# Kernel tuning notes

Measured on AMD Instinct MI355X. Metric: run time of the kernel, lower is better.

## Reference

```python
import jax, jax.numpy as jnp
import numpy as np

D_MODEL = 1024
D_STATE = 16
D_CONV = 4
EXPAND = 2
D_INNER = EXPAND * D_MODEL          # 2048
DT_RANK = (D_MODEL + 15) // 16      # 64 (mamba 'auto')
B, L = 2, 1024


def _mamba_params(key, scale=0.02):
    ks = jax.random.split(key, 6)
    return dict(
        inW=jax.random.normal(ks[0], (2 * D_INNER, D_MODEL), jnp.float32) * scale,
        convW=jax.random.normal(ks[1], (D_INNER, 1, D_CONV), jnp.float32) * scale,
        convb=jnp.zeros((D_INNER,), jnp.float32),
        xprojW=jax.random.normal(ks[2], (DT_RANK + 2 * D_STATE, D_INNER), jnp.float32) * scale,
        dtW=jax.random.normal(ks[3], (D_INNER, DT_RANK), jnp.float32) * scale,
        dtb=jax.random.normal(ks[4], (D_INNER,), jnp.float32) * scale,
        A_log=jnp.log(jnp.tile(jnp.arange(1, D_STATE + 1, dtype=jnp.float32), (D_INNER, 1))),
        Dskip=jnp.ones((D_INNER,), jnp.float32),
        outW=jax.random.normal(ks[5], (D_MODEL, D_INNER), jnp.float32) * scale,
    )


def setup_inputs() -> dict:
    key = jax.random.key(0)
    kx, kf, kb, kp = jax.random.split(key, 4)
    inp = {"x": jax.random.normal(kx, (B, L, D_MODEL), jnp.float32)}
    inp["ln_w"] = jnp.ones((D_MODEL,), jnp.float32)
    inp["ln_b"] = jnp.zeros((D_MODEL,), jnp.float32)
    for pref, k in (("f_", kf), ("b_", kb)):
        for name, v in _mamba_params(k).items():
            inp[pref + name] = v
    inp["proj_W"] = jax.random.normal(kp, (D_MODEL, 2 * D_MODEL), jnp.float32) * 0.02
    inp["proj_b"] = jnp.zeros((D_MODEL,), jnp.float32)
    return inp


def _layernorm(x, w, b, eps=1e-5):
    mu = jnp.mean(x, axis=-1, keepdims=True)
    var = jnp.var(x, axis=-1, keepdims=True)
    return (x - mu) * jax.lax.rsqrt(var + eps) * w + b


def _mamba(x, inW, convW, convb, xprojW, dtW, dtb, A_log, Dskip, outW):
    # x: [B, L, d_model]
    xz = jnp.einsum('bld,ed->ble', x, inW)           # [B,L,2*d_inner]
    xs, z = jnp.split(xz, 2, axis=-1)                # each [B,L,d_inner]
    # depthwise causal conv over L
    xc = jnp.transpose(xs, (0, 2, 1))                # [B,d_inner,L]
    xc = jax.lax.conv_general_dilated(
        xc, convW, window_strides=(1,), padding=[(D_CONV - 1, 0)],
        feature_group_count=D_INNER)
    xs = jax.nn.silu(jnp.transpose(xc + convb[None, :, None], (0, 2, 1)))
    # input-dependent dt, B, C
    xdb = jnp.einsum('bld,ed->ble', xs, xprojW)      # [B,L,dt_rank+2*d_state]
    dt, Bm, Cm = jnp.split(xdb, [DT_RANK, DT_RANK + D_STATE], axis=-1)
    dt = jax.nn.softplus(jnp.einsum('blr,dr->bld', dt, dtW) + dtb)  # [B,L,d_inner]
    A = -jnp.exp(A_log)                              # [d_inner,d_state], negative
    dA = jnp.exp(dt[..., None] * A)                  # [B,L,d_inner,d_state]
    dBx = dt[..., None] * Bm[:, :, None, :] * xs[..., None]

    def step(h, inputs):
        dA_t, dBx_t, C_t = inputs                    # [B,d,s],[B,d,s],[B,s]
        h = h * dA_t + dBx_t
        y = jnp.einsum('bds,bs->bd', h, C_t)
        return h, y

    h0 = jnp.zeros((x.shape[0], D_INNER, D_STATE), x.dtype)
    _, ys = jax.lax.scan(step, h0, (jnp.moveaxis(dA, 1, 0),
                                    jnp.moveaxis(dBx, 1, 0),
                                    jnp.moveaxis(Cm, 1, 0)))
    y = jnp.moveaxis(ys, 0, 1)                       # [B,L,d_inner]
    y = (y + xs * Dskip) * jax.nn.silu(z)
    return jnp.einsum('bld,ed->ble', y, outW)        # [B,L,d_model]


def reference(x, ln_w, ln_b,
              f_inW, f_convW, f_convb, f_xprojW, f_dtW, f_dtb, f_A_log, f_Dskip, f_outW,
              b_inW, b_convW, b_convb, b_xprojW, b_dtW, b_dtb, b_A_log, b_Dskip, b_outW,
              proj_W, proj_b):
    normed = _layernorm(x, ln_w, ln_b)
    fwd_out = _mamba(normed, f_inW, f_convW, f_convb, f_xprojW, f_dtW, f_dtb,
                     f_A_log, f_Dskip, f_outW)
    bwd_out = _mamba(normed[:, ::-1, :], b_inW, b_convW, b_convb, b_xprojW, b_dtW,
                     b_dtb, b_A_log, b_Dskip, b_outW)[:, ::-1, :]
    combined = jnp.concatenate([fwd_out, bwd_out], axis=-1)
    return x + jnp.einsum('blc,ec->ble', combined, proj_W) + proj_b
```

## Files before the change

### kernel.cpp

```cpp
#include <hip/hip_runtime.h>
#include <hip/hip_bf16.h>
#include <math.h>

#define DM   1024
#define DI   2048
#define DTR  64
#define DST  16
#define NB   2
#define LL   1024
#define MR   (NB*LL)
#define XLD  128
#define KS   8

typedef __bf16 bf16x8 __attribute__((ext_vector_type(8)));
typedef float  f32x4  __attribute__((ext_vector_type(4)));

__device__ __forceinline__ float siluf(float x) { return x / (1.f + __expf(-x)); }
__device__ __forceinline__ float softplusf(float x) {
    return fmaxf(x, 0.f) + log1pf(__expf(-fabsf(x)));
}
__device__ __forceinline__ unsigned short f2bf(float f) {
    __hip_bfloat16 h = __float2bfloat16(f);
    return *reinterpret_cast<unsigned short*>(&h);
}
__device__ __forceinline__ float bf2f(__hip_bfloat16 h) { return __bfloat162float(h); }

__device__ __forceinline__ void gl2lds16(const __hip_bfloat16* g, __hip_bfloat16* l)
{
    __builtin_amdgcn_global_load_lds(
        (const __attribute__((address_space(1))) unsigned int*)g,
        (__attribute__((address_space(3))) unsigned int*)l, 16, 0, 0);
}

__global__ __launch_bounds__(256) void prep_k(
    const float* __restrict__ s0, const float* __restrict__ s1,
    const float* __restrict__ s2, const float* __restrict__ s3,
    const float* __restrict__ s4, __hip_bfloat16* __restrict__ warena,
    const float* __restrict__ fx, const float* __restrict__ bx,
    __hip_bfloat16* __restrict__ wpb2,
    const float* __restrict__ fo, const float* __restrict__ bo,
    __hip_bfloat16* __restrict__ wot,
    const float* __restrict__ x, const float* __restrict__ lnw,
    const float* __restrict__ lnb, __hip_bfloat16* __restrict__ nb)
{
    __shared__ float pshm[64 * 65];
    const int b = blockIdx.x;
    const int tid = threadIdx.x;

    if (b < 10496) {
        long idx = (long)b * 1024 + tid * 4;
        const float* src; long off;
        if      (idx <  4194304L) { src = s0; off = idx; }
        else if (idx <  8388608L) { src = s1; off = idx -  4194304L; }
        else if (idx < 10485760L) { src = s2; off = idx -  8388608L; }
        else if (idx < 10616832L) { src = s3; off = idx - 10485760L; }
        else                      { src = s4; off = idx - 10616832L; }
        float4 v = *(const float4*)(src + off);
        ushort4 o;
        o.x = f2bf(v.x); o.y = f2bf(v.y); o.z = f2bf(v.z); o.w = f2bf(v.w);
        *(ushort4*)((unsigned short*)warena + idx) = o;
    } else if (b < 10624) {
        int t = b - 10496;
        int z = t >> 6;
        const float* in = z ? bx : fx;
        int idx = ((t & 63) * 256 + tid) * 4;
        int row = idx >> 11;
        ushort4 o = make_ushort4(0, 0, 0, 0);
        if (row < 96) {
            float4 v = *(const float4*)(in + idx);
            o.x = f2bf(v.x); o.y = f2bf(v.y); o.z = f2bf(v.z); o.w = f2bf(v.w);
        }
        *(ushort4*)((unsigned short*)wpb2 + (size_t)z * 128 * DI + idx) = o;
    } else if (b < 11648) {
        int t = b - 10624;
        int z = t >> 9; t &= 511;
        const float* src = z ? bo : fo;
        int c0 = (t & 31) * 64;
        int r0 = (t >> 5) * 64;
        int tc = tid & 63;
        int tr = tid >> 6;
        #pragma unroll
        for (int ii = 0; ii < 16; ++ii) {
            int rl = tr + ii * 4;
            pshm[tc * 65 + rl] = src[(size_t)(r0 + rl) * DI + c0 + tc];
        }
        __syncthreads();
        __hip_bfloat16* dst = wot + (size_t)z * DI * DM;
        #pragma unroll
        for (int ii = 0; ii < 16; ++ii) {
            int cl = tr + ii * 4;
            dst[(size_t)(c0 + cl) * DM + r0 + tc] = __float2bfloat16(pshm[cl * 65 + tc]);
        }
    } else {
        int row = b - 11648;
        const float* xr = x + (size_t)row * DM;
        float4 v = *(const float4*)(xr + tid * 4);
        float s = v.x + v.y + v.z + v.w;
        float q = v.x*v.x + v.y*v.y + v.z*v.z + v.w*v.w;
        #pragma unroll
        for (int off = 32; off > 0; off >>= 1) {
            s += __shfl_xor(s, off, 64);
            q += __shfl_xor(q, off, 64);
        }
        int wv = tid >> 6;
        if ((tid & 63) == 0) { pshm[wv] = s; pshm[8 + wv] = q; }
        __syncthreads();
        s = pshm[0] + pshm[1] + pshm[2] + pshm[3];
        q = pshm[8] + pshm[9] + pshm[10] + pshm[11];
        float mu  = s * (1.f / DM);
        float var = q * (1.f / DM) - mu * mu;
        float rstd = rsqrtf(var + 1e-5f);
        float4 wv4 = *(const float4*)(lnw + tid * 4);
        float4 bv4 = *(const float4*)(lnb + tid * 4);
        ushort4 o;
        o.x = f2bf((v.x - mu) * rstd * wv4.x + bv4.x);
        o.y = f2bf((v.y - mu) * rstd * wv4.y + bv4.y);
        o.z = f2bf((v.z - mu) * rstd * wv4.z + bv4.z);
        o.w = f2bf((v.w - mu) * rstd * wv4.w + bv4.w);
        *(ushort4*)((unsigned short*)nb + (size_t)row * DM + tid * 4) = o;
    }
}

template<int EPI>
__global__ __launch_bounds__(256) void gemm_gl(
    const __hip_bfloat16* __restrict__ A, int lda, size_t aofs,
    const __hip_bfloat16* __restrict__ B, int ldb, size_t bofs,
    void* __restrict__ Cp, int ldc, size_t cofs, int K,
    const float* __restrict__ bias0, const float* __restrict__ bias1)
{
    __shared__ __hip_bfloat16 smem[2 * 128 * 64];
    __hip_bfloat16* As = smem;
    __hip_bfloat16* Bs = smem + 128 * 64;
    const int tid  = threadIdx.x;
    const int z    = blockIdx.z;
    const int bm   = blockIdx.y * 128;
    const int bn   = blockIdx.x * 128;
    const __hip_bfloat16* Az = A + (size_t)z * aofs;
    const __hip_bfloat16* Bz = B + (size_t)z * bofs;
    const int wv   = tid >> 6;
    const int lane = tid & 63;
    const int wr   = (wv >> 1) * 64;
    const int wc   = (wv & 1) * 64;
    const int srow = wv * 32 + (lane >> 3);
    const int cg   = ((lane & 7) ^ (lane >> 3)) * 8;
    const int fr   = lane & 15;
    const int quad = lane >> 4;
    const int pc0  = (quad ^ (fr & 7)) * 8;
    const int pc1  = ((4 + quad) ^ (fr & 7)) * 8;

    f32x4 acc[4][4] = {};

    for (int k0 = 0; k0 < K; k0 += 64) {
        __syncthreads();
        #pragma unroll
        for (int i = 0; i < 4; ++i) {
            int r = srow + i * 8;
            gl2lds16(Az + (size_t)(bm + r) * lda + k0 + cg, As + wv * 2048 + i * 512);
            gl2lds16(Bz + (size_t)(bn + r) * ldb + k0 + cg, Bs + wv * 2048 + i * 512);
        }
        __syncthreads();
        #pragma unroll
        for (int kk = 0; kk < 2; ++kk) {
            const int pc = kk ? pc1 : pc0;
            bf16x8 af[4], bf_[4];
            #pragma unroll
            for (int i = 0; i < 4; ++i) {
                af[i]  = *(const bf16x8*)(As + (wr + i * 16 + fr) * 64 + pc);
                bf_[i] = *(const bf16x8*)(Bs + (wc + i * 16 + fr) * 64 + pc);
            }
            #pragma unroll
            for (int i = 0; i < 4; ++i)
                #pragma unroll
                for (int j = 0; j < 4; ++j)
                    acc[i][j] = __builtin_amdgcn_mfma_f32_16x16x32_bf16(
                        af[i], bf_[j], acc[i][j], 0, 0, 0);
        }
    }

    const float* bias = (EPI == 3) ? (z ? bias1 : bias0) : nullptr;
    float* eps = (float*)smem;
    const int half = wv >> 1;
    const int lrow = tid >> 3;
    const int cseg = (tid & 7) * 16;
    const int gr_  = bm + (lrow >> 4) * 64 + (lrow & 15);
    #pragma unroll
    for (int i = 0; i < 4; ++i) {
        __syncthreads();
        #pragma unroll
        for (int j = 0; j < 4; ++j)
            #pragma unroll
            for (int r = 0; r < 4; ++r)
                eps[(half * 16 + quad * 4 + r) * 132 + wc + j * 16 + fr] = acc[i][j][r];
        __syncthreads();
        float vals[16];
        *(float4*)(vals +  0) = *(const float4*)(eps + lrow * 132 + cseg +  0);
        *(float4*)(vals +  4) = *(const float4*)(eps + lrow * 132 + cseg +  4);
        *(float4*)(vals +  8) = *(const float4*)(eps + lrow * 132 + cseg +  8);
        *(float4*)(vals + 12) = *(const float4*)(eps + lrow * 132 + cseg + 12);
        int gr = gr_ + i * 16;
        int gc = bn + cseg;
        if (EPI == 0) {
            float* dst = (float*)Cp + (size_t)z * cofs + (size_t)gr * ldc + gc;
            *(float4*)(dst +  0) = *(const float4*)(vals +  0);
            *(float4*)(dst +  4) = *(const float4*)(vals +  4);
            *(float4*)(dst +  8) = *(const float4*)(vals +  8);
            *(float4*)(dst + 12) = *(const float4*)(vals + 12);
        } else {
            unsigned short os[16];
            #pragma unroll
            for (int c = 0; c < 16; ++c) {
                float t = vals[c];
                if (EPI == 3) t = softplusf(t + bias[gc + c]);
                os[c] = f2bf(t);
            }
            unsigned short* dst = (unsigned short*)Cp + (size_t)z * cofs +
                                  (size_t)gr * ldc + gc;
            *(ushort4*)(dst +  0) = *(ushort4*)(os +  0);
            *(ushort4*)(dst +  4) = *(ushort4*)(os +  4);
            *(ushort4*)(dst +  8) = *(ushort4*)(os +  8);
            *(ushort4*)(dst + 12) = *(ushort4*)(os + 12);
        }
    }
}

__global__ __launch_bounds__(256) void xproj_part_k(
    const __hip_bfloat16* __restrict__ A,
    const __hip_bfloat16* __restrict__ B,
    float* __restrict__ part)
{
    __shared__ __hip_bfloat16 smem[2 * 128 * 64];
    __hip_bfloat16* As = smem;
    __hip_bfloat16* Bs = smem + 128 * 64;
    const int tid  = threadIdx.x;
    const int ks   = blockIdx.x;
    const int bm   = blockIdx.y * 128;
    const int z    = blockIdx.z;
    const __hip_bfloat16* Az = A + (size_t)z * MR * DI;
    const __hip_bfloat16* Bz = B + (size_t)z * 128 * DI;
    const int kb   = ks * (DI / KS);
    const int wv   = tid >> 6;
    const int lane = tid & 63;
    const int wr   = (wv >> 1) * 64;
    const int wc   = (wv & 1) * 64;
    const int srow = wv * 32 + (lane >> 3);
    const int cg   = ((lane & 7) ^ (lane >> 3)) * 8;
    const int fr   = lane & 15;
    const int quad = lane >> 4;
    const int pc0  = (quad ^ (fr & 7)) * 8;
    const int pc1  = ((4 + quad) ^ (fr & 7)) * 8;

    f32x4 acc[4][4] = {};

    #pragma unroll
    for (int k0 = 0; k0 < DI / KS; k0 += 64) {
        __syncthreads();
        #pragma unroll
        for (int i = 0; i < 4; ++i) {
            int r = srow + i * 8;
            gl2lds16(Az + (size_t)(bm + r) * DI + kb + k0 + cg, As + wv * 2048 + i * 512);
            gl2lds16(Bz + (size_t)r * DI + kb + k0 + cg,        Bs + wv * 2048 + i * 512);
        }
        __syncthreads();
        #pragma unroll
        for (int kk = 0; kk < 2; ++kk) {
            const int pc = kk ? pc1 : pc0;
            bf16x8 af[4], bf_[4];
            #pragma unroll
            for (int i = 0; i < 4; ++i) {
                af[i]  = *(const bf16x8*)(As + (wr + i * 16 + fr) * 64 + pc);
                bf_[i] = *(const bf16x8*)(Bs + (wc + i * 16 + fr) * 64 + pc);
            }
            #pragma unroll
            for (int i = 0; i < 4; ++i)
                #pragma unroll
                for (int j = 0; j < 4; ++j)
                    acc[i][j] = __builtin_amdgcn_mfma_f32_16x16x32_bf16(
                        af[i], bf_[j], acc[i][j], 0, 0, 0);
        }
    }

    float* dst = part + ((size_t)z * KS + ks) * MR * XLD;
    const int er = quad * 4;
    #pragma unroll
    for (int i = 0; i < 4; ++i)
        #pragma unroll
        for (int j = 0; j < 4; ++j) {
            int row = bm + wr + i * 16 + er;
            int col = wc + j * 16 + fr;
            #pragma unroll
            for (int r = 0; r < 4; ++r)
                dst[(size_t)(row + r) * XLD + col] = acc[i][j][r];
        }
}

__global__ __launch_bounds__(256) void xproj_reduce_k(
    const float* __restrict__ part, float* __restrict__ xdb,
    __hip_bfloat16* __restrict__ xdbt)
{
    int z = blockIdx.y;
    size_t idx = ((size_t)blockIdx.x * 256 + threadIdx.x) * 4;
    const float* p = part + (size_t)z * KS * MR * XLD;
    float4 s = make_float4(0.f, 0.f, 0.f, 0.f);
    #pragma unroll
    for (int ks = 0; ks < KS; ++ks) {
        float4 v = *(const float4*)(p + (size_t)ks * MR * XLD + idx);
        s.x += v.x; s.y += v.y; s.z += v.z; s.w += v.w;
    }
    *(float4*)(xdb + (size_t)z * MR * XLD + idx) = s;
    int c = (int)(idx & (XLD - 1));
    if (c < 64) {
        size_t m = idx >> 7;
        ushort4 o;
        o.x = f2bf(s.x); o.y = f2bf(s.y); o.z = f2bf(s.z); o.w = f2bf(s.w);
        *(ushort4*)((unsigned short*)xdbt + (size_t)z * MR * 64 + m * 64 + c) = o;
    }
}

__global__ __launch_bounds__(256) void conv_silu_k(
    const __hip_bfloat16* __restrict__ xz2,
    const float* __restrict__ fW, const float* __restrict__ fb,
    const float* __restrict__ bW, const float* __restrict__ bb_,
    __hip_bfloat16* __restrict__ xsb2)
{
    int dirv = blockIdx.y;
    int idx = blockIdx.x * 256 + threadIdx.x;
    int d = idx & (DI - 1);
    int m = idx >> 11;
    int t = m & (LL - 1);
    int bb = m >> 10;
    const float* w  = (dirv ? bW : fW) + d * 4;
    const __hip_bfloat16* xz = xz2 + (size_t)dirv * MR * 2 * DI;
    float acc = (dirv ? bb_ : fb)[d];
    if (dirv == 0) {
        #pragma unroll
        for (int k = 0; k < 4; ++k) {
            int tt = t - 3 + k;
            if (tt >= 0)
                acc = fmaf(w[k], bf2f(xz[(size_t)(bb * LL + tt) * (2 * DI) + d]), acc);
        }
    } else {
        #pragma unroll
        for (int k = 0; k < 4; ++k) {
            int tt = t + 3 - k;
            if (tt < LL)
                acc = fmaf(w[k], bf2f(xz[(size_t)(bb * LL + tt) * (2 * DI) + d]), acc);
        }
    }
    xsb2[(size_t)dirv * MR * DI + (size_t)m * DI + d] = __float2bfloat16(siluf(acc));
}

__global__ __launch_bounds__(256) void scan1_k(
    const __hip_bfloat16* __restrict__ dtf2, const __hip_bfloat16* __restrict__ xsb2,
    const float* __restrict__ xdb2,
    const float* __restrict__ fA, const float* __restrict__ bA,
    float* __restrict__ hend, float* __restrict__ aprod, int G, int Cn)
{
    int d  = blockIdx.x * 256 + threadIdx.x;
    int bb = blockIdx.y;
    int zz = blockIdx.z;
    int dirv = (zz >= G) ? 1 : 0;
    int g = zz - (dirv ? G : 0);
    const float* A_log = dirv ? bA : fA;
    const __hip_bfloat16* dtf = dtf2 + (size_t)dirv * MR * DI;
    const __hip_bfloat16* xs = xsb2 + (size_t)dirv * MR * DI;
    const float* xdb = xdb2 + (size_t)dirv * MR * XLD;
    size_t hoff = (size_t)dirv * G * (NB * DI * DST);

    float Ad[DST], h[DST], ap[DST];
    bool pw = true;
    #pragma unroll
    for (int s = 0; s < DST; ++s) {
        Ad[s] = -__expf(A_log[d * DST + s]);
        pw = pw && (fabsf(Ad[s] + (float)(s + 1)) < 1e-3f * (s + 1));
        h[s] = 0.f; ap[s] = 1.f;
    }
    int i0 = g * Cn;
    for (int i = 0; i < Cn; ++i) {
        int ii = i0 + i;
        int t = dirv ? (LL - 1 - ii) : ii;
        size_t m = (size_t)bb * LL + t;
        float dtv = bf2f(dtf[m * DI + d]);
        float xv  = bf2f(xs[m * DI + d]);
        const float* bc = xdb + m * XLD;
        float dtx = dtv * xv;
        float dAv[DST];
        if (pw) {
            float r = __expf(-dtv);
            float a = r;
            #pragma unroll
            for (int s = 0; s < DST; ++s) { dAv[s] = a; a *= r; }
        } else {
            #pragma unroll
            for (int s = 0; s < DST; ++s) dAv[s] = __expf(dtv * Ad[s]);
        }
        #pragma unroll
        for (int s = 0; s < DST; ++s) {
            h[s] = fmaf(h[s], dAv[s], dtx * bc[64 + s]);
            ap[s] *= dAv[s];
        }
    }
    size_t base = hoff + ((size_t)(g * NB + bb) * DI + d) * DST;
    #pragma unroll
    for (int s = 0; s < DST; s += 4) {
        *(float4*)(hend  + base + s) = make_float4(h[s], h[s+1], h[s+2], h[s+3]);
        *(float4*)(aprod + base + s) = make_float4(ap[s], ap[s+1], ap[s+2], ap[s+3]);
    }
}

__global__ __launch_bounds__(256) void scan2_k(
    float* __restrict__ hend, const float* __restrict__ aprod, int G)
{
    int dirv = blockIdx.y;
    int idx = blockIdx.x * 256 + threadIdx.x;
    const int slab = NB * DI * DST;
    size_t hoff = (size_t)dirv * G * slab;
    float carry = 0.f;
    for (int g = 0; g < G; ++g) {
        size_t off = hoff + (size_t)g * slab + idx;
        float a = aprod[off];
        float e = hend[off];
        hend[off] = carry;
        carry = fmaf(a, carry, e);
    }
}

__global__ __launch_bounds__(256) void scan3_k(
    const __hip_bfloat16* __restrict__ dtf2, const __hip_bfloat16* __restrict__ xsb2,
    const float* __restrict__ xdb2, const __hip_bfloat16* __restrict__ xz2,
    const float* __restrict__ fA, const float* __restrict__ bA,
    const float* __restrict__ fD, const float* __restrict__ bD,
    const float* __restrict__ hin, __hip_bfloat16* __restrict__ ycat, int G, int Cn)
{
    int d  = blockIdx.x * 256 + threadIdx.x;
    int bb = blockIdx.y;
    int zz = blockIdx.z;
    int dirv = (zz >= G) ? 1 : 0;
    int g = zz - (dirv ? G : 0);
    const float* A_log = dirv ? bA : fA;
    const float* Dskip = dirv ? bD : fD;
    const __hip_bfloat16* dtf = dtf2 + (size_t)dirv * MR * DI;
    const __hip_bfloat16* xs = xsb2 + (size_t)dirv * MR * DI;
    const float* xdb = xdb2 + (size_t)dirv * MR * XLD;
    const __hip_bfloat16* xz = xz2 + (size_t)dirv * MR * 2 * DI;
    size_t hoff = (size_t)dirv * G * (NB * DI * DST);

    float Ad[DST], h[DST];
    bool pw = true;
    size_t base = hoff + ((size_t)(g * NB + bb) * DI + d) * DST;
    #pragma unroll
    for (int s = 0; s < DST; ++s) {
        Ad[s] = -__expf(A_log[d * DST + s]);
        pw = pw && (fabsf(Ad[s] + (float)(s + 1)) < 1e-3f * (s + 1));
        h[s] = hin[base + s];
    }
    float Dsk = Dskip[d];
    int i0 = g * Cn;
    for (int i = 0; i < Cn; ++i) {
        int ii = i0 + i;
        int t = dirv ? (LL - 1 - ii) : ii;
        size_t m = (size_t)bb * LL + t;
        float dtv = bf2f(dtf[m * DI + d]);
        float xv  = bf2f(xs[m * DI + d]);
        const float* bc = xdb + m * XLD;
        float dtx = dtv * xv;
        float dAv[DST];
        if (pw) {
            float r = __expf(-dtv);
            float a = r;
            #pragma unroll
            for (int s = 0; s < DST; ++s) { dAv[s] = a; a *= r; }
        } else {
            #pragma unroll
            for (int s = 0; s < DST; ++s) dAv[s] = __expf(dtv * Ad[s]);
        }
        float yv = 0.f;
        #pragma unroll
        for (int s = 0; s < DST; ++s) {
            h[s] = fmaf(h[s], dAv[s], dtx * bc[64 + s]);
            yv = fmaf(h[s], bc[80 + s], yv);
        }
        float zv = bf2f(xz[m * (2 * DI) + DI + d]);
        ycat[m * (2 * DI) + (size_t)dirv * DI + d] =
            __float2bfloat16((yv + xv * Dsk) * siluf(zv));
    }
}

__global__ __launch_bounds__(256) void scan_mono_k(
    const __hip_bfloat16* __restrict__ dtf2, const __hip_bfloat16* __restrict__ xsb2,
    const float* __restrict__ xdb2, const __hip_bfloat16* __restrict__ xz2,
    const float* __restrict__ fA, const float* __restrict__ bA,
    const float* __restrict__ fD, const float* __restrict__ bD,
    __hip_bfloat16* __restrict__ ycat)
{
    int d  = blockIdx.x * 256 + threadIdx.x;
    int bb = blockIdx.y;
    int dirv = blockIdx.z;
    const float* A_log = dirv ? bA : fA;
    const float* Dskip = dirv ? bD : fD;
    const __hip_bfloat16* dtf = dtf2 + (size_t)dirv * MR * DI;
    const __hip_bfloat16* xs = xsb2 + (size_t)dirv * MR * DI;
    const float* xdb = xdb2 + (size_t)dirv * MR * XLD;
    const __hip_bfloat16* xz = xz2 + (size_t)dirv * MR * 2 * DI;
    float Ad[DST], h[DST];
    #pragma unroll
    for (int s = 0; s < DST; ++s) { Ad[s] = -__expf(A_log[d * DST + s]); h[s] = 0.f; }
    float Dsk = Dskip[d];
    for (int i = 0; i < LL; ++i) {
        int t = dirv ? (LL - 1 - i) : i;
        size_t m = (size_t)bb * LL + t;
        float dtv = bf2f(dtf[m * DI + d]);
        float xv  = bf2f(xs[m * DI + d]);
        const float* bc = xdb + m * XLD;
        float dtx = dtv * xv;
        float yv = 0.f;
        #pragma unroll
        for (int s = 0; s < DST; ++s) {
            float dA = __expf(dtv * Ad[s]);
            h[s] = fmaf(h[s], dA, dtx * bc[64 + s]);
            yv = fmaf(h[s], bc[80 + s], yv);
        }
        float zv = bf2f(xz[m * (2 * DI) + DI + d]);
        ycat[m * (2 * DI) + (size_t)dirv * DI + d] =
            __float2bfloat16((yv + xv * Dsk) * siluf(zv));
    }
}

__global__ __launch_bounds__(256) void final_reduce_k(
    const float* __restrict__ part, const float* __restrict__ x,
    const float* __restrict__ proj_b, float* __restrict__ out)
{
    size_t idx = ((size_t)blockIdx.x * 256 + threadIdx.x) * 4;
    float4 s = make_float4(0.f, 0.f, 0.f, 0.f);
    #pragma unroll
    for (int z = 0; z < 4; ++z) {
        float4 v = *(const float4*)(part + (size_t)z * MR * DM + idx);
        s.x += v.x; s.y += v.y; s.z += v.z; s.w += v.w;
    }
    float4 xv = *(const float4*)(x + idx);
    float4 pb = *(const float4*)(proj_b + (idx & (DM - 1)));
    float4 o;
    o.x = xv.x + pb.x + s.x;
    o.y = xv.y + pb.y + s.y;
    o.z = xv.z + pb.z + s.z;
    o.w = xv.w + pb.w + s.w;
    *(float4*)(out + idx) = o;
}

extern "C" void kernel_launch(void* const* d_in, const int* in_sizes, int n_in,
                              void* d_out, int out_size, void* d_ws, size_t ws_size,
                              hipStream_t stream)
{
    const float* x      = (const float*)d_in[0];
    const float* ln_w   = (const float*)d_in[1];
    const float* ln_b   = (const float*)d_in[2];
    const float* f_inW    = (const float*)d_in[3];
    const float* f_convW  = (const float*)d_in[4];
    const float* f_convb  = (const float*)d_in[5];
    const float* f_xprojW = (const float*)d_in[6];
    const float* f_dtW    = (const float*)d_in[7];
    const float* f_dtb    = (const float*)d_in[8];
    const float* f_A_log  = (const float*)d_in[9];
    const float* f_Dskip  = (const float*)d_in[10];
    const float* f_outW   = (const float*)d_in[11];
    const float* b_inW    = (const float*)d_in[12];
    const float* b_convW  = (const float*)d_in[13];
    const float* b_convb  = (const float*)d_in[14];
    const float* b_xprojW = (const float*)d_in[15];
    const float* b_dtW    = (const float*)d_in[16];
    const float* b_dtb    = (const float*)d_in[17];
    const float* b_A_log  = (const float*)d_in[18];
    const float* b_Dskip  = (const float*)d_in[19];
    const float* b_outW   = (const float*)d_in[20];
    const float* proj_W = (const float*)d_in[21];
    const float* proj_b = (const float*)d_in[22];

    float* ws = (float*)d_ws;
    size_t o = 0;
    __hip_bfloat16* xz2  = (__hip_bfloat16*)(ws + o);
    __hip_bfloat16* wot  = xz2;
    float* fpart = ws + o;
    o += (size_t)2 * MR * 2 * DI / 2;
    __hip_bfloat16* xsb2 = (__hip_bfloat16*)(ws + o); o += (size_t)2 * MR * DI / 2;
    __hip_bfloat16* ycat = (__hip_bfloat16*)(ws + o);
    float* xpart = ws + o;
    o += (size_t)MR * 2 * DI / 2;
    float* xdb2 = ws + o; o += (size_t)2 * MR * XLD;
    __hip_bfloat16* xdbt = (__hip_bfloat16*)(ws + o); o += (size_t)2 * MR * 64 / 2;
    __hip_bfloat16* dtfb = (__hip_bfloat16*)(ws + o); o += (size_t)2 * MR * DI / 2;
    __hip_bfloat16* nb = (__hip_bfloat16*)(ws + o); o += (size_t)MR * DM / 2;
    __hip_bfloat16* warena = (__hip_bfloat16*)(ws + o); o += 15466496 / 2;
    float* hbuf = ws + o;
    size_t base_floats = o;

    __hip_bfloat16* wbi  = warena;
    __hip_bfloat16* pwb  = warena +  8388608;
    __hip_bfloat16* wdt  = warena + 10485760;
    __hip_bfloat16* wpb2 = warena + 10747904;
    __hip_bfloat16* wcat = warena + 11272192;

    const size_t slab = (size_t)NB * DI * DST;
    int G = 32;
    while (G > 4 && (base_floats + 4ull * G * slab) * 4 > ws_size) G >>= 1;
    int useChunks = ((base_floats + 4ull * G * slab) * 4 <= ws_size);
    float* hend  = hbuf;
    float* aprod = hbuf + 2ull * G * slab;
    int Cn = useChunks ? LL / G : LL;

    prep_k<<<13696, 256, 0, stream>>>(
        f_inW, b_inW, proj_W, f_dtW, b_dtW, warena,
        f_xprojW, b_xprojW, wpb2,
        f_outW, b_outW, wot,
        x, ln_w, ln_b, nb);

    gemm_gl<1><<<dim3(DI / 128, DM / 128, 2), 256, 0, stream>>>(
        pwb, 2 * DM, (size_t)DM, wot, DM, (size_t)DI * DM,
        wcat, 2 * DI, (size_t)DI, DM, nullptr, nullptr);

    gemm_gl<1><<<dim3((2 * DI) / 128, MR / 128, 2), 256, 0, stream>>>(
        nb, DM, 0, wbi, DM, (size_t)2 * DI * DM,
        xz2, 2 * DI, (size_t)MR * 2 * DI, DM, nullptr, nullptr);

    conv_silu_k<<<dim3((MR * DI) / 256, 2), 256, 0, stream>>>(
        xz2, f_convW, f_convb, b_convW, b_convb, xsb2);

    xproj_part_k<<<dim3(KS, MR / 128, 2), 256, 0, stream>>>(xsb2, wpb2, xpart);
    xproj_reduce_k<<<dim3((MR * XLD) / 1024, 2), 256, 0, stream>>>(xpart, xdb2, xdbt);

    gemm_gl<3><<<dim3(DI / 128, MR / 128, 2), 256, 0, stream>>>(
        xdbt, 64, (size_t)MR * 64, wdt, 64, (size_t)DI * 64,
        dtfb, DI, (size_t)MR * DI, 64, f_dtb, b_dtb);

    if (useChunks) {
        scan1_k<<<dim3(DI / 256, NB, 2 * G), 256, 0, stream>>>(
            dtfb, xsb2, xdb2, f_A_log, b_A_log, hend, aprod, G, Cn);
        scan2_k<<<dim3((NB * DI * DST) / 256, 2), 256, 0, stream>>>(hend, aprod, G);
        scan3_k<<<dim3(DI / 256, NB, 2 * G), 256, 0, stream>>>(
            dtfb, xsb2, xdb2, xz2, f_A_log, b_A_log, f_Dskip, b_Dskip,
            hend, ycat, G, Cn);
    } else {
        scan_mono_k<<<dim3(DI / 256, NB, 2), 256, 0, stream>>>(
            dtfb, xsb2, xdb2, xz2, f_A_log, b_A_log, f_Dskip, b_Dskip, ycat);
    }

    gemm_gl<0><<<dim3(DM / 128, MR / 128, 4), 256, 0, stream>>>(
        ycat, 2 * DI, 1024, wcat, 2 * DI, 1024,
        fpart, DM, (size_t)MR * DM, 1024, nullptr, nullptr);

    final_reduce_k<<<(MR * DM) / 1024, 256, 0, stream>>>(
        fpart, x, proj_b, (float*)d_out);
}
```

Before: 422.6 us.

## Fuse post-prep pipeline into one cooperative persistent kernel with grid syncs

Replaces the sequence of separate kernel launches (in-proj and weight-combine GEMMs, conv, x-proj split-K and reduce, dt GEMM, three scan phases, output GEMM and reduce) with a single cooperative persistent kernel that loops over virtual blocks and uses grid.sync between stages. The aim is to remove per-launch overhead and the idle gaps between dependent kernels. The in-proj GEMM and the weight-combine GEMM now run in the same stage, and the wot buffer is moved into hbuf so the two can run together. The cost is a grid capped at 512 blocks, so the scan phases and small stages may be underparallelised, plus the overhead of the grid barriers themselves. A fallback multi-kernel path that uses a fused inproj_wcat kernel is kept.

Result: slower. 900.3 us (+113.0%).

```diff
diff --git a/kernel.cpp b/kernel.cpp
--- a/kernel.cpp
+++ b/kernel.cpp
@@ -1,6 +1,9 @@
 #include <hip/hip_runtime.h>
 #include <hip/hip_bf16.h>
+#include <hip/hip_cooperative_groups.h>
 #include <math.h>
+
+namespace cg = cooperative_groups;
 
 #define DM   1024
 #define DI   2048
@@ -24,12 +27,321 @@
     return *reinterpret_cast<unsigned short*>(&h);
 }
 __device__ __forceinline__ float bf2f(__hip_bfloat16 h) { return __bfloat162float(h); }
+__device__ __forceinline__ float u2f(unsigned short u) {
+    return __uint_as_float(((unsigned int)u) << 16);
+}
 
 __device__ __forceinline__ void gl2lds16(const __hip_bfloat16* g, __hip_bfloat16* l)
 {
     __builtin_amdgcn_global_load_lds(
         (const __attribute__((address_space(1))) unsigned int*)g,
         (__attribute__((address_space(3))) unsigned int*)l, 16, 0, 0);
+}
+
+
+template<int EPI>
+__device__ __forceinline__ void gemm_tile(
+    __hip_bfloat16* smem, int tid,
+    const __hip_bfloat16* __restrict__ Az, int lda,
+    const __hip_bfloat16* __restrict__ Bz, int ldb,
+    void* __restrict__ Cz, int ldc, int K,
+    int bm, int bn, const float* __restrict__ bias)
+{
+    __hip_bfloat16* As = smem;
+    __hip_bfloat16* Bs = smem + 128 * 64;
+    const int wv   = tid >> 6;
+    const int lane = tid & 63;
+    const int wr   = (wv >> 1) * 64;
+    const int wc   = (wv & 1) * 64;
+    const int srow = wv * 32 + (lane >> 3);
+    const int cg_  = ((lane & 7) ^ (lane >> 3)) * 8;
+    const int fr   = lane & 15;
+    const int quad = lane >> 4;
+    const int pc0  = (quad ^ (fr & 7)) * 8;
+    const int pc1  = ((4 + quad) ^ (fr & 7)) * 8;
+
+    f32x4 acc[4][4] = {};
+
+    for (int k0 = 0; k0 < K; k0 += 64) {
+        __syncthreads();
+        #pragma unroll
+        for (int i = 0; i < 4; ++i) {
+            int r = srow + i * 8;
+            gl2lds16(Az + (size_t)(bm + r) * lda + k0 + cg_, As + wv * 2048 + i * 512);
+            gl2lds16(Bz + (size_t)(bn + r) * ldb + k0 + cg_, Bs + wv * 2048 + i * 512);
+        }
+        __syncthreads();
+        #pragma unroll
+        for (int kk = 0; kk < 2; ++kk) {
+            const int pc = kk ? pc1 : pc0;
+            bf16x8 af[4], bf_[4];
+            #pragma unroll
+            for (int i = 0; i < 4; ++i) {
+                af[i]  = *(const bf16x8*)(As + (wr + i * 16 + fr) * 64 + pc);
+                bf_[i] = *(const bf16x8*)(Bs + (wc + i * 16 + fr) * 64 + pc);
+            }
+            #pragma unroll
+            for (int i = 0; i < 4; ++i)
+                #pragma unroll
+                for (int j = 0; j < 4; ++j)
+                    acc[i][j] = __builtin_amdgcn_mfma_f32_16x16x32_bf16(
+                        af[i], bf_[j], acc[i][j], 0, 0, 0);
+        }
+    }
+
+    float* eps = (float*)smem;
+    const int half = wv >> 1;
+    const int lrow = tid >> 3;
+    const int cseg = (tid & 7) * 16;
+    const int gr_  = bm + (lrow >> 4) * 64 + (lrow & 15);
+    #pragma unroll
+    for (int i = 0; i < 4; ++i) {
+        __syncthreads();
+        #pragma unroll
+        for (int j = 0; j < 4; ++j)
+            #pragma unroll
+            for (int r = 0; r < 4; ++r)
+                eps[(half * 16 + quad * 4 + r) * 132 + wc + j * 16 + fr] = acc[i][j][r];
+        __syncthreads();
+        float vals[16];
+        *(float4*)(vals +  0) = *(const float4*)(eps + lrow * 132 + cseg +  0);
+        *(float4*)(vals +  4) = *(const float4*)(eps + lrow * 132 + cseg +  4);
+        *(float4*)(vals +  8) = *(const float4*)(eps + lrow * 132 + cseg +  8);
+        *(float4*)(vals + 12) = *(const float4*)(eps + lrow * 132 + cseg + 12);
+        int gr = gr_ + i * 16;
+        int gc = bn + cseg;
+        if (EPI == 0) {
+            float* dst = (float*)Cz + (size_t)gr * ldc + gc;
+            *(float4*)(dst +  0) = *(const float4*)(vals +  0);
+            *(float4*)(dst +  4) = *(const float4*)(vals +  4);
+            *(float4*)(dst +  8) = *(const float4*)(vals +  8);
+            *(float4*)(dst + 12) = *(const float4*)(vals + 12);
+        } else {
+            unsigned short os[16];
+            #pragma unroll
+            for (int c = 0; c < 16; ++c) {
+                float t = vals[c];
+                if (EPI == 3) t = softplusf(t + bias[gc + c]);
+                os[c] = f2bf(t);
+            }
+            unsigned short* dst = (unsigned short*)Cz + (size_t)gr * ldc + gc;
+            *(ushort4*)(dst +  0) = *(ushort4*)(os +  0);
+            *(ushort4*)(dst +  4) = *(ushort4*)(os +  4);
+            *(ushort4*)(dst +  8) = *(ushort4*)(os +  8);
+            *(ushort4*)(dst + 12) = *(ushort4*)(os + 12);
+        }
+    }
+}
+
+__device__ __forceinline__ void conv_body(
+    int q, const __hip_bfloat16* __restrict__ xz2,
+    const float* __restrict__ fW, const float* __restrict__ fb,
+    const float* __restrict__ bW, const float* __restrict__ bb_,
+    __hip_bfloat16* __restrict__ xsb2)
+{
+    const int TQH = MR * DI / 4;
+    int dirv = q >= TQH;
+    int mq = q - (dirv ? TQH : 0);
+    int m = mq >> 9;
+    int d = (mq & 511) << 2;
+    int t = m & (LL - 1);
+    int bb = m >> 10;
+    const float* W  = (dirv ? bW : fW) + d * 4;
+    const float* Bp = (dirv ? bb_ : fb) + d;
+    const __hip_bfloat16* xz = xz2 + (size_t)dirv * MR * 2 * DI;
+    float4 bi = *(const float4*)Bp;
+    float acc0 = bi.x, acc1 = bi.y, acc2 = bi.z, acc3 = bi.w;
+    float w_[16];
+    *(float4*)(w_ + 0)  = *(const float4*)(W + 0);
+    *(float4*)(w_ + 4)  = *(const float4*)(W + 4);
+    *(float4*)(w_ + 8)  = *(const float4*)(W + 8);
+    *(float4*)(w_ + 12) = *(const float4*)(W + 12);
+    #pragma unroll
+    for (int k = 0; k < 4; ++k) {
+        int tt = dirv ? (t + 3 - k) : (t - 3 + k);
+        bool ok = dirv ? (tt < LL) : (tt >= 0);
+        if (ok) {
+            ushort4 xv = *(const ushort4*)((const unsigned short*)xz +
+                         (size_t)(bb * LL + tt) * 2 * DI + d);
+            acc0 = fmaf(w_[0 + k],  u2f(xv.x), acc0);
+            acc1 = fmaf(w_[4 + k],  u2f(xv.y), acc1);
+            acc2 = fmaf(w_[8 + k],  u2f(xv.z), acc2);
+            acc3 = fmaf(w_[12 + k], u2f(xv.w), acc3);
+        }
+    }
+    ushort4 o;
+    o.x = f2bf(siluf(acc0)); o.y = f2bf(siluf(acc1));
+    o.z = f2bf(siluf(acc2)); o.w = f2bf(siluf(acc3));
+    *(ushort4*)((unsigned short*)xsb2 + (size_t)dirv * MR * DI +
+                (size_t)m * DI + d) = o;
+}
+
+__device__ __forceinline__ void xreduce_body(
+    size_t idx, int z, const float* __restrict__ part,
+    float* __restrict__ xdb, __hip_bfloat16* __restrict__ xdbt)
+{
+    const float* p = part + (size_t)z * KS * MR * XLD;
+    float4 s = make_float4(0.f, 0.f, 0.f, 0.f);
+    #pragma unroll
+    for (int ks = 0; ks < KS; ++ks) {
+        float4 v = *(const float4*)(p + (size_t)ks * MR * XLD + idx);
+        s.x += v.x; s.y += v.y; s.z += v.z; s.w += v.w;
+    }
+    *(float4*)(xdb + (size_t)z * MR * XLD + idx) = s;
+    int c = (int)(idx & (XLD - 1));
+    if (c < 64) {
+        size_t m = idx >> 7;
+        ushort4 o;
+        o.x = f2bf(s.x); o.y = f2bf(s.y); o.z = f2bf(s.z); o.w = f2bf(s.w);
+        *(ushort4*)((unsigned short*)xdbt + (size_t)z * MR * 64 + m * 64 + c) = o;
+    }
+}
+
+__device__ __forceinline__ void scan1_body(
+    int d, int bb, int dirv, int g, int G, int Cn,
+    const __hip_bfloat16* __restrict__ dtf2, const __hip_bfloat16* __restrict__ xsb2,
+    const float* __restrict__ xdb2,
+    const float* __restrict__ fA, const float* __restrict__ bA,
+    float* __restrict__ hend, float* __restrict__ aprod)
+{
+    const float* A_log = dirv ? bA : fA;
+    const __hip_bfloat16* dtf = dtf2 + (size_t)dirv * MR * DI;
+    const __hip_bfloat16* xs = xsb2 + (size_t)dirv * MR * DI;
+    const float* xdb = xdb2 + (size_t)dirv * MR * XLD;
+    size_t hoff = (size_t)dirv * G * (NB * DI * DST);
+
+    float Ad[DST], h[DST], ap[DST];
+    bool pw = true;
+    #pragma unroll
+    for (int s = 0; s < DST; ++s) {
+        Ad[s] = -__expf(A_log[d * DST + s]);
+        pw = pw && (fabsf(Ad[s] + (float)(s + 1)) < 1e-3f * (s + 1));
+        h[s] = 0.f; ap[s] = 1.f;
+    }
+    int i0 = g * Cn;
+    for (int i = 0; i < Cn; ++i) {
+        int ii = i0 + i;
+        int t = dirv ? (LL - 1 - ii) : ii;
+        size_t m = (size_t)bb * LL + t;
+        float dtv = bf2f(dtf[m * DI + d]);
+        float xv  = bf2f(xs[m * DI + d]);
+        const float* bc = xdb + m * XLD;
+        float dtx = dtv * xv;
+        float dAv[DST];
+        if (pw) {
+            float r = __expf(-dtv);
+            float a = r;
+            #pragma unroll
+            for (int s = 0; s < DST; ++s) { dAv[s] = a; a *= r; }
+        } else {
+            #pragma unroll
+            for (int s = 0; s < DST; ++s) dAv[s] = __expf(dtv * Ad[s]);
+        }
+        #pragma unroll
+        for (int s = 0; s < DST; ++s) {
+            h[s] = fmaf(h[s], dAv[s], dtx * bc[64 + s]);
+            ap[s] *= dAv[s];
+        }
+    }
+    size_t base = hoff + ((size_t)(g * NB + bb) * DI + d) * DST;
+    #pragma unroll
+    for (int s = 0; s < DST; s += 4) {
+        *(float4*)(hend  + base + s) = make_float4(h[s], h[s+1], h[s+2], h[s+3]);
+        *(float4*)(aprod + base + s) = make_float4(ap[s], ap[s+1], ap[s+2], ap[s+3]);
+    }
+}
+
+__device__ __forceinline__ void scan2_body(
+    int idx, int dirv, float* __restrict__ hend,
+    const float* __restrict__ aprod, int G)
+{
+    const int slab = NB * DI * DST;
+    size_t hoff = (size_t)dirv * G * slab;
+    float carry = 0.f;
+    for (int g = 0; g < G; ++g) {
+        size_t off = hoff + (size_t)g * slab + idx;
+        float a = aprod[off];
+        float e = hend[off];
+        hend[off] = carry;
+        carry = fmaf(a, carry, e);
+    }
+}
+
+__device__ __forceinline__ void scan3_body(
+    int d, int bb, int dirv, int g, int G, int Cn,
+    const __hip_bfloat16* __restrict__ dtf2, const __hip_bfloat16* __restrict__ xsb2,
+    const float* __restrict__ xdb2, const __hip_bfloat16* __restrict__ xz2,
+    const float* __restrict__ fA, const float* __restrict__ bA,
+    const float* __restrict__ fD, const float* __restrict__ bD,
+    const float* __restrict__ hin, __hip_bfloat16* __restrict__ ycat)
+{
+    const float* A_log = dirv ? bA : fA;
+    const float* Dskip = dirv ? bD : fD;
+    const __hip_bfloat16* dtf = dtf2 + (size_t)dirv * MR * DI;
+    const __hip_bfloat16* xs = xsb2 + (size_t)dirv * MR * DI;
+    const float* xdb = xdb2 + (size_t)dirv * MR * XLD;
+    const __hip_bfloat16* xz = xz2 + (size_t)dirv * MR * 2 * DI;
+    size_t hoff = (size_t)dirv * G * (NB * DI * DST);
+
+    float Ad[DST], h[DST];
+    bool pw = true;
+    size_t base = hoff + ((size_t)(g * NB + bb) * DI + d) * DST;
+    #pragma unroll
+    for (int s = 0; s < DST; ++s) {
+        Ad[s] = -__expf(A_log[d * DST + s]);
+        pw = pw && (fabsf(Ad[s] + (float)(s + 1)) < 1e-3f * (s + 1));
+        h[s] = hin[base + s];
+    }
+    float Dsk = Dskip[d];
+    int i0 = g * Cn;
+    for (int i = 0; i < Cn; ++i) {
+        int ii = i0 + i;
+        int t = dirv ? (LL - 1 - ii) : ii;
+        size_t m = (size_t)bb * LL + t;
+        float dtv = bf2f(dtf[m * DI + d]);
+        float xv  = bf2f(xs[m * DI + d]);
+        const float* bc = xdb + m * XLD;
+        float dtx = dtv * xv;
+        float dAv[DST];
+        if (pw) {
+            float r = __expf(-dtv);
+            float a = r;
+            #pragma unroll
+            for (int s = 0; s < DST; ++s) { dAv[s] = a; a *= r; }
+        } else {
+            #pragma unroll
+            for (int s = 0; s < DST; ++s) dAv[s] = __expf(dtv * Ad[s]);
+        }
+        float yv = 0.f;
+        #pragma unroll
+        for (int s = 0; s < DST; ++s) {
+            h[s] = fmaf(h[s], dAv[s], dtx * bc[64 + s]);
+            yv = fmaf(h[s], bc[80 + s], yv);
+        }
+        float zv = bf2f(xz[m * (2 * DI) + DI + d]);
+        ycat[m * (2 * DI) + (size_t)dirv * DI + d] =
+            __float2bfloat16((yv + xv * Dsk) * siluf(zv));
+    }
+}
+
+__device__ __forceinline__ void freduce_body(
+    size_t idx, const float* __restrict__ part, const float* __restrict__ x,
+    const float* __restrict__ proj_b, float* __restrict__ out)
+{
+    float4 s = make_float4(0.f, 0.f, 0.f, 0.f);
+    #pragma unroll
+    for (int z = 0; z < 4; ++z) {
+        float4 v = *(const float4*)(part + (size_t)z * MR * DM + idx);
+        s.x += v.x; s.y += v.y; s.z += v.z; s.w += v.w;
+    }
+    float4 xv = *(const float4*)(x + idx);
+    float4 pb = *(const float4*)(proj_b + (idx & (DM - 1)));
+    float4 o;
+    o.x = xv.x + pb.x + s.x;
+    o.y = xv.y + pb.y + s.y;
+    o.z = xv.z + pb.z + s.z;
+    o.w = xv.w + pb.w + s.w;
+    *(float4*)(out + idx) = o;
 }
 
 __global__ __launch_bounds__(256) void prep_k(
@@ -121,6 +433,114 @@
     }
 }
 
+struct MegaArgs {
+    const __hip_bfloat16 *nb, *wbi, *pwb, *wot, *wpb2, *wdt;
+    __hip_bfloat16 *xz2, *wcat, *xsb2, *xdbt, *dtfb, *ycat;
+    const float *fW, *fb, *bW, *bb_;
+    float *xpart, *xdb2;
+    const float *fdtb, *bdtb, *fA, *bA, *fD, *bD;
+    float *hend, *aprod;
+    const float *x, *proj_b;
+    float *fpart, *outp;
+    int G, Cn;
+};
+
+__global__ __launch_bounds__(256, 2) void mega_k(MegaArgs P)
+{
+    __shared__ __hip_bfloat16 smem[2 * 128 * 64];
+    cg::grid_group grid = cg::this_grid();
+    const int tid = threadIdx.x;
+    const int bid = blockIdx.x;
+    const int gsz = gridDim.x;
+
+    for (int vb = bid; vb < 1280; vb += gsz) {
+        const __hip_bfloat16 *Az, *Bz; __hip_bfloat16* Cz; int lda, bm, bn;
+        if (vb < 1024) {
+            int zz = vb >> 9, rem = vb & 511;
+            bm = (rem >> 5) * 128; bn = (rem & 31) * 128;
+            Az = P.nb; lda = DM;
+            Bz = P.wbi + (size_t)zz * 2 * DI * DM;
+            Cz = P.xz2 + (size_t)zz * MR * 2 * DI;
+        } else {
+            int w = vb - 1024; int zc = w >> 7, rem = w & 127;
+            bm = (rem >> 4) * 128; bn = (rem & 15) * 128;
+            Az = P.pwb + (size_t)zc * DM; lda = 2 * DM;
+            Bz = P.wot + (size_t)zc * DI * DM;
+            Cz = P.wcat + (size_t)zc * DI;
+        }
+        gemm_tile<1>(smem, tid, Az, lda, Bz, DM, Cz, 2 * DI, DM, bm, bn, nullptr);
+    }
+    grid.sync();
+
+    for (int vb = bid; vb < 8192; vb += gsz)
+        conv_body(vb * 256 + tid, P.xz2, P.fW, P.fb, P.bW, P.bb_, P.xsb2);
+    grid.sync();
+
+    for (int vb = bid; vb < 256; vb += gsz) {
+        int ks = vb & 7, byv = (vb >> 3) & 15, z = vb >> 7;
+        int kb = ks * (DI / KS);
+        gemm_tile<0>(smem, tid,
+            P.xsb2 + (size_t)z * MR * DI + kb, DI,
+            P.wpb2 + (size_t)z * 128 * DI + kb, DI,
+            P.xpart + ((size_t)z * KS + ks) * MR * XLD, XLD,
+            DI / KS, byv * 128, 0, nullptr);
+    }
+    grid.sync();
+
+    for (int vb = bid; vb < 512; vb += gsz)
+        xreduce_body(((size_t)(vb & 255) * 256 + tid) * 4, vb >> 8,
+                     P.xpart, P.xdb2, P.xdbt);
+    grid.sync();
+
+    for (int vb = bid; vb < 512; vb += gsz) {
+        int z = vb >> 8, rem = vb & 255;
+        int bm = (rem >> 4) * 128, bn = (rem & 15) * 128;
+        gemm_tile<3>(smem, tid,
+            P.xdbt + (size_t)z * MR * 64, 64,
+            P.wdt + (size_t)z * DI * 64, 64,
+            P.dtfb + (size_t)z * MR * DI, DI,
+            64, bm, bn, z ? P.bdtb : P.fdtb);
+    }
+    grid.sync();
+
+    for (int vb = bid; vb < 32 * P.G; vb += gsz) {
+        int zz = vb >> 4, bb = (vb >> 3) & 1, bx = vb & 7;
+        int dirv = (zz >= P.G) ? 1 : 0;
+        int g = zz - (dirv ? P.G : 0);
+        scan1_body(bx * 256 + tid, bb, dirv, g, P.G, P.Cn,
+                   P.dtfb, P.xsb2, P.xdb2, P.fA, P.bA, P.hend, P.aprod);
+    }
+    grid.sync();
+
+    for (int vb = bid; vb < 512; vb += gsz)
+        scan2_body((vb & 255) * 256 + tid, vb >> 8, P.hend, P.aprod, P.G);
+    grid.sync();
+
+    for (int vb = bid; vb < 32 * P.G; vb += gsz) {
+        int zz = vb >> 4, bb = (vb >> 3) & 1, bx = vb & 7;
+        int dirv = (zz >= P.G) ? 1 : 0;
+        int g = zz - (dirv ? P.G : 0);
+        scan3_body(bx * 256 + tid, bb, dirv, g, P.G, P.Cn,
+                   P.dtfb, P.xsb2, P.xdb2, P.xz2, P.fA, P.bA, P.fD, P.bD,
+                   P.hend, P.ycat);
+    }
+    grid.sync();
+
+    for (int vb = bid; vb < 512; vb += gsz) {
+        int z = vb >> 7, rem = vb & 127;
+        int bm = (rem >> 3) * 128, bn = (rem & 7) * 128;
+        gemm_tile<0>(smem, tid,
+            P.ycat + (size_t)z * 1024, 2 * DI,
+            P.wcat + (size_t)z * 1024, 2 * DI,
+            P.fpart + (size_t)z * MR * DM, DM,
+            1024, bm, bn, nullptr);
+    }
+    grid.sync();
+
+    for (int vb = bid; vb < 2048; vb += gsz)
+        freduce_body(((size_t)vb * 256 + tid) * 4, P.fpart, P.x, P.proj_b, P.outp);
+}
+
 template<int EPI>
 __global__ __launch_bounds__(256) void gemm_gl(
     const __hip_bfloat16* __restrict__ A, int lda, size_t aofs,
@@ -129,98 +549,38 @@
     const float* __restrict__ bias0, const float* __restrict__ bias1)
 {
     __shared__ __hip_bfloat16 smem[2 * 128 * 64];
-    __hip_bfloat16* As = smem;
-    __hip_bfloat16* Bs = smem + 128 * 64;
-    const int tid  = threadIdx.x;
-    const int z    = blockIdx.z;
-    const int bm   = blockIdx.y * 128;
-    const int bn   = blockIdx.x * 128;
-    const __hip_bfloat16* Az = A + (size_t)z * aofs;
-    const __hip_bfloat16* Bz = B + (size_t)z * bofs;
-    const int wv   = tid >> 6;
-    const int lane = tid & 63;
-    const int wr   = (wv >> 1) * 64;
-    const int wc   = (wv & 1) * 64;
-    const int srow = wv * 32 + (lane >> 3);
-    const int cg   = ((lane & 7) ^ (lane >> 3)) * 8;
-    const int fr   = lane & 15;
-    const int quad = lane >> 4;
-    const int pc0  = (quad ^ (fr & 7)) * 8;
-    const int pc1  = ((4 + quad) ^ (fr & 7)) * 8;
-
-    f32x4 acc[4][4] = {};
-
-    for (int k0 = 0; k0 < K; k0 += 64) {
-        __syncthreads();
-        #pragma unroll
-        for (int i = 0; i < 4; ++i) {
-            int r = srow + i * 8;
-            gl2lds16(Az + (size_t)(bm + r) * lda + k0 + cg, As + wv * 2048 + i * 512);
-            gl2lds16(Bz + (size_t)(bn + r) * ldb + k0 + cg, Bs + wv * 2048 + i * 512);
-        }
-        __syncthreads();
-        #pragma unroll
-        for (int kk = 0; kk < 2; ++kk) {
-            const int pc = kk ? pc1 : pc0;
-            bf16x8 af[4], bf_[4];
-            #pragma unroll
-            for (int i = 0; i < 4; ++i) {
-                af[i]  = *(const bf16x8*)(As + (wr + i * 16 + fr) * 64 + pc);
-                bf_[i] = *(const bf16x8*)(Bs + (wc + i * 16 + fr) * 64 + pc);
-            }
-            #pragma unroll
-            for (int i = 0; i < 4; ++i)
-                #pragma unroll
-                for (int j = 0; j < 4; ++j)
-                    acc[i][j] = __builtin_amdgcn_mfma_f32_16x16x32_bf16(
-                        af[i], bf_[j], acc[i][j], 0, 0, 0);
-        }
-    }
-
-    const float* bias = (EPI == 3) ? (z ? bias1 : bias0) : nullptr;
-    float* eps = (float*)smem;
-    const int half = wv >> 1;
-    const int lrow = tid >> 3;
-    const int cseg = (tid & 7) * 16;
-    const int gr_  = bm + (lrow >> 4) * 64 + (lrow & 15);
-    #pragma unroll
-    for (int i = 0; i < 4; ++i) {
-        __syncthreads();
-        #pragma unroll
-        for (int j = 0; j < 4; ++j)
-            #pragma unroll
-            for (int r = 0; r < 4; ++r)
-                eps[(half * 16 + quad * 4 + r) * 132 + wc + j * 16 + fr] = acc[i][j][r];
-        __syncthreads();
-        float vals[16];
-        *(float4*)(vals +  0) = *(const float4*)(eps + lrow * 132 + cseg +  0);
-        *(float4*)(vals +  4) = *(const float4*)(eps + lrow * 132 + cseg +  4);
-        *(float4*)(vals +  8) = *(const float4*)(eps + lrow * 132 + cseg +  8);
-        *(float4*)(vals + 12) = *(const float4*)(eps + lrow * 132 + cseg + 12);
-        int gr = gr_ + i * 16;
-        int gc = bn + cseg;
-        if (EPI == 0) {
-            float* dst = (float*)Cp + (size_t)z * cofs + (size_t)gr * ldc + gc;
-            *(float4*)(dst +  0) = *(const float4*)(vals +  0);
-            *(float4*)(dst +  4) = *(const float4*)(vals +  4);
-            *(float4*)(dst +  8) = *(const float4*)(vals +  8);
-            *(float4*)(dst + 12) = *(const float4*)(vals + 12);
-        } else {
-            unsigned short os[16];
-            #pragma unroll
-            for (int c = 0; c < 16; ++c) {
-                float t = vals[c];
-                if (EPI == 3) t = softplusf(t + bias[gc + c]);
-                os[c] = f2bf(t);
-            }
-            unsigned short* dst = (unsigned short*)Cp + (size_t)z * cofs +
-                                  (size_t)gr * ldc + gc;
-            *(ushort4*)(dst +  0) = *(ushort4*)(os +  0);
-            *(ushort4*)(dst +  4) = *(ushort4*)(os +  4);
-            *(ushort4*)(dst +  8) = *(ushort4*)(os +  8);
-            *(ushort4*)(dst + 12) = *(ushort4*)(os + 12);
-        }
-    }
+    const int z = blockIdx.z;
+    void* Cz;
+    if (EPI == 0) Cz = (float*)Cp + (size_t)z * cofs;
+    else          Cz = (__hip_bfloat16*)Cp + (size_t)z * cofs;
+    gemm_tile<EPI>(smem, threadIdx.x,
+        A + (size_t)z * aofs, lda, B + (size_t)z * bofs, ldb,
+        Cz, ldc, K, blockIdx.y * 128, blockIdx.x * 128,
+        (EPI == 3) ? (z ? bias1 : bias0) : nullptr);
+}
+
+__global__ __launch_bounds__(256) void inproj_wcat_k(
+    const __hip_bfloat16* __restrict__ nb,  const __hip_bfloat16* __restrict__ wbi,
+    __hip_bfloat16* __restrict__ xz2,
+    const __hip_bfloat16* __restrict__ pwb, const __hip_bfloat16* __restrict__ wot,
+    __hip_bfloat16* __restrict__ wcat)
+{
+    __shared__ __hip_bfloat16 smem[2 * 128 * 64];
+    const int z = blockIdx.z;
+    const int bxv = blockIdx.x, byv = blockIdx.y;
+    if (z >= 2 && (bxv >= 16 || byv >= 8)) return;
+    const __hip_bfloat16 *Az, *Bz; __hip_bfloat16* Cz; int lda;
+    if (z < 2) {
+        Az = nb; lda = DM;
+        Bz = wbi + (size_t)z * 2 * DI * DM;
+        Cz = xz2 + (size_t)z * MR * 2 * DI;
+    } else {
+        Az = pwb + (size_t)(z - 2) * DM; lda = 2 * DM;
+        Bz = wot + (size_t)(z - 2) * DI * DM;
+        Cz = wcat + (size_t)(z - 2) * DI;
+    }
+    gemm_tile<1>(smem, threadIdx.x, Az, lda, Bz, DM, Cz, 2 * DI, DM,
+                 byv * 128, bxv * 128, nullptr);
 }
 
 __global__ __launch_bounds__(256) void xproj_part_k(
@@ -229,91 +589,21 @@
     float* __restrict__ part)
 {
     __shared__ __hip_bfloat16 smem[2 * 128 * 64];
-    __hip_bfloat16* As = smem;
-    __hip_bfloat16* Bs = smem + 128 * 64;
-    const int tid  = threadIdx.x;
-    const int ks   = blockIdx.x;
-    const int bm   = blockIdx.y * 128;
-    const int z    = blockIdx.z;
-    const __hip_bfloat16* Az = A + (size_t)z * MR * DI;
-    const __hip_bfloat16* Bz = B + (size_t)z * 128 * DI;
-    const int kb   = ks * (DI / KS);
-    const int wv   = tid >> 6;
-    const int lane = tid & 63;
-    const int wr   = (wv >> 1) * 64;
-    const int wc   = (wv & 1) * 64;
-    const int srow = wv * 32 + (lane >> 3);
-    const int cg   = ((lane & 7) ^ (lane >> 3)) * 8;
-    const int fr   = lane & 15;
-    const int quad = lane >> 4;
-    const int pc0  = (quad ^ (fr & 7)) * 8;
-    const int pc1  = ((4 + quad) ^ (fr & 7)) * 8;
-
-    f32x4 acc[4][4] = {};
-
-    #pragma unroll
-    for (int k0 = 0; k0 < DI / KS; k0 += 64) {
-        __syncthreads();
-        #pragma unroll
-        for (int i = 0; i < 4; ++i) {
-            int r = srow + i * 8;
-            gl2lds16(Az + (size_t)(bm + r) * DI + kb + k0 + cg, As + wv * 2048 + i * 512);
-            gl2lds16(Bz + (size_t)r * DI + kb + k0 + cg,        Bs + wv * 2048 + i * 512);
-        }
-        __syncthreads();
-        #pragma unroll
-        for (int kk = 0; kk < 2; ++kk) {
-            const int pc = kk ? pc1 : pc0;
-            bf16x8 af[4], bf_[4];
-            #pragma unroll
-            for (int i = 0; i < 4; ++i) {
-                af[i]  = *(const bf16x8*)(As + (wr + i * 16 + fr) * 64 + pc);
-                bf_[i] = *(const bf16x8*)(Bs + (wc + i * 16 + fr) * 64 + pc);
-            }
-            #pragma unroll
-            for (int i = 0; i < 4; ++i)
-                #pragma unroll
-                for (int j = 0; j < 4; ++j)
-                    acc[i][j] = __builtin_amdgcn_mfma_f32_16x16x32_bf16(
-                        af[i], bf_[j], acc[i][j], 0, 0, 0);
-        }
-    }
-
-    float* dst = part + ((size_t)z * KS + ks) * MR * XLD;
-    const int er = quad * 4;
-    #pragma unroll
-    for (int i = 0; i < 4; ++i)
-        #pragma unroll
-        for (int j = 0; j < 4; ++j) {
-            int row = bm + wr + i * 16 + er;
-            int col = wc + j * 16 + fr;
-            #pragma unroll
-            for (int r = 0; r < 4; ++r)
-                dst[(size_t)(row + r) * XLD + col] = acc[i][j][r];
-        }
+    const int ks = blockIdx.x, z = blockIdx.z;
+    const int kb = ks * (DI / KS);
+    gemm_tile<0>(smem, threadIdx.x,
+        A + (size_t)z * MR * DI + kb, DI,
+        B + (size_t)z * 128 * DI + kb, DI,
+        part + ((size_t)z * KS + ks) * MR * XLD, XLD,
+        DI / KS, blockIdx.y * 128, 0, nullptr);
 }
 
 __global__ __launch_bounds__(256) void xproj_reduce_k(
     const float* __restrict__ part, float* __restrict__ xdb,
     __hip_bfloat16* __restrict__ xdbt)
 {
-    int z = blockIdx.y;
-    size_t idx = ((size_t)blockIdx.x * 256 + threadIdx.x) * 4;
-    const float* p = part + (size_t)z * KS * MR * XLD;
-    float4 s = make_float4(0.f, 0.f, 0.f, 0.f);
-    #pragma unroll
-    for (int ks = 0; ks < KS; ++ks) {
-        float4 v = *(const float4*)(p + (size_t)ks * MR * XLD + idx);
-        s.x += v.x; s.y += v.y; s.z += v.z; s.w += v.w;
-    }
-    *(float4*)(xdb + (size_t)z * MR * XLD + idx) = s;
-    int c = (int)(idx & (XLD - 1));
-    if (c < 64) {
-        size_t m = idx >> 7;
-        ushort4 o;
-        o.x = f2bf(s.x); o.y = f2bf(s.y); o.z = f2bf(s.z); o.w = f2bf(s.w);
-        *(ushort4*)((unsigned short*)xdbt + (size_t)z * MR * 64 + m * 64 + c) = o;
-    }
+    xreduce_body(((size_t)blockIdx.x * 256 + threadIdx.x) * 4, blockIdx.y,
+                 part, xdb, xdbt);
 }
 
 __global__ __launch_bounds__(256) void conv_silu_k(
@@ -322,31 +612,7 @@
     const float* __restrict__ bW, const float* __restrict__ bb_,
     __hip_bfloat16* __restrict__ xsb2)
 {
-    int dirv = blockIdx.y;
-    int idx = blockIdx.x * 256 + threadIdx.x;
-    int d = idx & (DI - 1);
-    int m = idx >> 11;
-    int t = m & (LL - 1);
-    int bb = m >> 10;
-    const float* w  = (dirv ? bW : fW) + d * 4;
-    const __hip_bfloat16* xz = xz2 + (size_t)dirv * MR * 2 * DI;
-    float acc = (dirv ? bb_ : fb)[d];
-    if (dirv == 0) {
-        #pragma unroll
-        for (int k = 0; k < 4; ++k) {
-            int tt = t - 3 + k;
-            if (tt >= 0)
-                acc = fmaf(w[k], bf2f(xz[(size_t)(bb * LL + tt) * (2 * DI) + d]), acc);
-        }
-    } else {
-        #pragma unroll
-        for (int k = 0; k < 4; ++k) {
-            int tt = t + 3 - k;
-            if (tt < LL)
-                acc = fmaf(w[k], bf2f(xz[(size_t)(bb * LL + tt) * (2 * DI) + d]), acc);
-        }
-    }
-    xsb2[(size_t)dirv * MR * DI + (size_t)m * DI + d] = __float2bfloat16(siluf(acc));
+    conv_body(blockIdx.x * 256 + threadIdx.x, xz2, fW, fb, bW, bb_, xsb2);
 }
 
 __global__ __launch_bounds__(256) void scan1_k(
@@ -355,73 +621,16 @@
     const float* __restrict__ fA, const float* __restrict__ bA,
     float* __restrict__ hend, float* __restrict__ aprod, int G, int Cn)
 {
-    int d  = blockIdx.x * 256 + threadIdx.x;
-    int bb = blockIdx.y;
     int zz = blockIdx.z;
     int dirv = (zz >= G) ? 1 : 0;
-    int g = zz - (dirv ? G : 0);
-    const float* A_log = dirv ? bA : fA;
-    const __hip_bfloat16* dtf = dtf2 + (size_t)dirv * MR * DI;
-    const __hip_bfloat16* xs = xsb2 + (size_t)dirv * MR * DI;
-    const float* xdb = xdb2 + (size_t)dirv * MR * XLD;
-    size_t hoff = (size_t)dirv * G * (NB * DI * DST);
-
-    float Ad[DST], h[DST], ap[DST];
-    bool pw = true;
-    #pragma unroll
-    for (int s = 0; s < DST; ++s) {
-        Ad[s] = -__expf(A_log[d * DST + s]);
-        pw = pw && (fabsf(Ad[s] + (float)(s + 1)) < 1e-3f * (s + 1));
-        h[s] = 0.f; ap[s] = 1.f;
-    }
-    int i0 = g * Cn;
-    for (int i = 0; i < Cn; ++i) {
-        int ii = i0 + i;
-        int t = dirv ? (LL - 1 - ii) : ii;
-        size_t m = (size_t)bb * LL + t;
-        float dtv = bf2f(dtf[m * DI + d]);
-        float xv  = bf2f(xs[m * DI + d]);
-        const float* bc = xdb + m * XLD;
-        float dtx = dtv * xv;
-        float dAv[DST];
-        if (pw) {
-            float r = __expf(-dtv);
-            float a = r;
-            #pragma unroll
-            for (int s = 0; s < DST; ++s) { dAv[s] = a; a *= r; }
-        } else {
-            #pragma unroll
-            for (int s = 0; s < DST; ++s) dAv[s] = __expf(dtv * Ad[s]);
-        }
-        #pragma unroll
-        for (int s = 0; s < DST; ++s) {
-            h[s] = fmaf(h[s], dAv[s], dtx * bc[64 + s]);
-            ap[s] *= dAv[s];
-        }
-    }
-    size_t base = hoff + ((size_t)(g * NB + bb) * DI + d) * DST;
-    #pragma unroll
-    for (int s = 0; s < DST; s += 4) {
-        *(float4*)(hend  + base + s) = make_float4(h[s], h[s+1], h[s+2], h[s+3]);
-        *(float4*)(aprod + base + s) = make_float4(ap[s], ap[s+1], ap[s+2], ap[s+3]);
-    }
+    scan1_body(blockIdx.x * 256 + threadIdx.x, blockIdx.y, dirv,
+               zz - (dirv ? G : 0), G, Cn, dtf2, xsb2, xdb2, fA, bA, hend, aprod);
 }
 
 __global__ __launch_bounds__(256) void scan2_k(
     float* __restrict__ hend, const float* __restrict__ aprod, int G)
 {
-    int dirv = blockIdx.y;
-    int idx = blockIdx.x * 256 + threadIdx.x;
-    const int slab = NB * DI * DST;
-    size_t hoff = (size_t)dirv * G * slab;
-    float carry = 0.f;
-    for (int g = 0; g < G; ++g) {
-        size_t off = hoff + (size_t)g * slab + idx;
-        float a = aprod[off];
-        float e = hend[off];
-        hend[off] = carry;
-        carry = fmaf(a, carry, e);
-    }
+    scan2_body(blockIdx.x * 256 + threadIdx.x, blockIdx.y, hend, aprod, G);
 }
 
 __global__ __launch_bounds__(256) void scan3_k(
@@ -431,58 +640,11 @@
     const float* __restrict__ fD, const float* __restrict__ bD,
     const float* __restrict__ hin, __hip_bfloat16* __restrict__ ycat, int G, int Cn)
 {
-    int d  = blockIdx.x * 256 + threadIdx.x;
-    int bb = blockIdx.y;
     int zz = blockIdx.z;
     int dirv = (zz >= G) ? 1 : 0;
-    int g = zz - (dirv ? G : 0);
-    const float* A_log = dirv ? bA : fA;
-    const float* Dskip = dirv ? bD : fD;
-    const __hip_bfloat16* dtf = dtf2 + (size_t)dirv * MR * DI;
-    const __hip_bfloat16* xs = xsb2 + (size_t)dirv * MR * DI;
-    const float* xdb = xdb2 + (size_t)dirv * MR * XLD;
-    const __hip_bfloat16* xz = xz2 + (size_t)dirv * MR * 2 * DI;
-    size_t hoff = (size_t)dirv * G * (NB * DI * DST);
-
-    float Ad[DST], h[DST];
-    bool pw = true;
-    size_t base = hoff + ((size_t)(g * NB + bb) * DI + d) * DST;
-    #pragma unroll
-    for (int s = 0; s < DST; ++s) {
-        Ad[s] = -__expf(A_log[d * DST + s]);
-        pw = pw && (fabsf(Ad[s] + (float)(s + 1)) < 1e-3f * (s + 1));
-        h[s] = hin[base + s];
-    }
-    float Dsk = Dskip[d];
-    int i0 = g * Cn;
-    for (int i = 0; i < Cn; ++i) {
-        int ii = i0 + i;
-        int t = dirv ? (LL - 1 - ii) : ii;
-        size_t m = (size_t)bb * LL + t;
-        float dtv = bf2f(dtf[m * DI + d]);
-        float xv  = bf2f(xs[m * DI + d]);
-        const float* bc = xdb + m * XLD;
-        float dtx = dtv * xv;
-        float dAv[DST];
-        if (pw) {
-            float r = __expf(-dtv);
-            float a = r;
-            #pragma unroll
-            for (int s = 0; s < DST; ++s) { dAv[s] = a; a *= r; }
-        } else {
-            #pragma unroll
-            for (int s = 0; s < DST; ++s) dAv[s] = __expf(dtv * Ad[s]);
-        }
-        float yv = 0.f;
-        #pragma unroll
-        for (int s = 0; s < DST; ++s) {
-            h[s] = fmaf(h[s], dAv[s], dtx * bc[64 + s]);
-            yv = fmaf(h[s], bc[80 + s], yv);
-        }
-        float zv = bf2f(xz[m * (2 * DI) + DI + d]);
-        ycat[m * (2 * DI) + (size_t)dirv * DI + d] =
-            __float2bfloat16((yv + xv * Dsk) * siluf(zv));
-    }
+    scan3_body(blockIdx.x * 256 + threadIdx.x, blockIdx.y, dirv,
+               zz - (dirv ? G : 0), G, Cn, dtf2, xsb2, xdb2, xz2,
+               fA, bA, fD, bD, hin, ycat);
 }
 
 __global__ __launch_bounds__(256) void scan_mono_k(
@@ -529,21 +691,7 @@
     const float* __restrict__ part, const float* __restrict__ x,
     const float* __restrict__ proj_b, float* __restrict__ out)
 {
-    size_t idx = ((size_t)blockIdx.x * 256 + threadIdx.x) * 4;
-    float4 s = make_float4(0.f, 0.f, 0.f, 0.f);
-    #pragma unroll
-    for (int z = 0; z < 4; ++z) {
-        float4 v = *(const float4*)(part + (size_t)z * MR * DM + idx);
-        s.x += v.x; s.y += v.y; s.z += v.z; s.w += v.w;
-    }
-    float4 xv = *(const float4*)(x + idx);
-    float4 pb = *(const float4*)(proj_b + (idx & (DM - 1)));
-    float4 o;
-    o.x = xv.x + pb.x + s.x;
-    o.y = xv.y + pb.y + s.y;
-    o.z = xv.z + pb.z + s.z;
-    o.w = xv.w + pb.w + s.w;
-    *(float4*)(out + idx) = o;
+    freduce_body(((size_t)blockIdx.x * 256 + threadIdx.x) * 4, part, x, proj_b, out);
 }
 
 extern "C" void kernel_launch(void* const* d_in, const int* in_sizes, int n_in,
@@ -577,7 +725,6 @@
     float* ws = (float*)d_ws;
     size_t o = 0;
     __hip_bfloat16* xz2  = (__hip_bfloat16*)(ws + o);
-    __hip_bfloat16* wot  = xz2;
     float* fpart = ws + o;
     o += (size_t)2 * MR * 2 * DI / 2;
     __hip_bfloat16* xsb2 = (__hip_bfloat16*)(ws + o); o += (size_t)2 * MR * DI / 2;
@@ -606,21 +753,54 @@
     float* aprod = hbuf + 2ull * G * slab;
     int Cn = useChunks ? LL / G : LL;
 
+    int wotInHbuf = useChunks && (4ull * G * slab >= 2097152ull);
+    __hip_bfloat16* wot = wotInHbuf ? (__hip_bfloat16*)hbuf : xz2;
+
+    int coop = 0;
+    hipDeviceGetAttribute(&coop, hipDeviceAttributeCooperativeLaunch, 0);
+    int occ = 0;
+    if (coop) hipOccupancyMaxActiveBlocksPerMultiprocessor(&occ, mega_k, 256, 0);
+    int gsz = occ * 256; if (gsz > 512) gsz = 512;
+    bool mega_ok = useChunks && wotInHbuf && coop && gsz >= 256;
+
     prep_k<<<13696, 256, 0, stream>>>(
         f_inW, b_inW, proj_W, f_dtW, b_dtW, warena,
         f_xprojW, b_xprojW, wpb2,
         f_outW, b_outW, wot,
         x, ln_w, ln_b, nb);
 
-    gemm_gl<1><<<dim3(DI / 128, DM / 128, 2), 256, 0, stream>>>(
-        pwb, 2 * DM, (size_t)DM, wot, DM, (size_t)DI * DM,
-        wcat, 2 * DI, (size_t)DI, DM, nullptr, nullptr);
-
-    gemm_gl<1><<<dim3((2 * DI) / 128, MR / 128, 2), 256, 0, stream>>>(
-        nb, DM, 0, wbi, DM, (size_t)2 * DI * DM,
-        xz2, 2 * DI, (size_t)MR * 2 * DI, DM, nullptr, nullptr);
-
-    conv_silu_k<<<dim3((MR * DI) / 256, 2), 256, 0, stream>>>(
+    if (mega_ok) {
+        MegaArgs ma;
+        ma.nb = nb; ma.wbi = wbi; ma.pwb = pwb; ma.wot = wot;
+        ma.wpb2 = wpb2; ma.wdt = wdt;
+        ma.xz2 = xz2; ma.wcat = wcat; ma.xsb2 = xsb2; ma.xdbt = xdbt;
+        ma.dtfb = dtfb; ma.ycat = ycat;
+        ma.fW = f_convW; ma.fb = f_convb; ma.bW = b_convW; ma.bb_ = b_convb;
+        ma.xpart = xpart; ma.xdb2 = xdb2;
+        ma.fdtb = f_dtb; ma.bdtb = b_dtb;
+        ma.fA = f_A_log; ma.bA = b_A_log; ma.fD = f_Dskip; ma.bD = b_Dskip;
+        ma.hend = hend; ma.aprod = aprod;
+        ma.x = x; ma.proj_b = proj_b;
+        ma.fpart = fpart; ma.outp = (float*)d_out;
+        ma.G = G; ma.Cn = Cn;
+        void* kp[] = { &ma };
+        hipError_t e = hipLaunchCooperativeKernel(
+            mega_k, dim3(gsz), dim3(256), kp, 0, stream);
+        if (e == hipSuccess) return;
+    }
+
+    if (wotInHbuf) {
+        inproj_wcat_k<<<dim3(32, 16, 4), 256, 0, stream>>>(
+            nb, wbi, xz2, pwb, wot, wcat);
+    } else {
+        gemm_gl<1><<<dim3(DI / 128, DM / 128, 2), 256, 0, stream>>>(
+            pwb, 2 * DM, (size_t)DM, wot, DM, (size_t)DI * DM,
+            wcat, 2 * DI, (size_t)DI, DM, nullptr, nullptr);
+        inproj_wcat_k<<<dim3(32, 16, 2), 256, 0, stream>>>(
+            nb, wbi, xz2, pwb, wot, wcat);
+    }
+
+    conv_silu_k<<<8192, 256, 0, stream>>>(
         xz2, f_convW, f_convb, b_convW, b_convb, xsb2);
 
     xproj_part_k<<<dim3(KS, MR / 128, 2), 256, 0, stream>>>(xsb2, wpb2, xpart);
```
